# Kernel optimization log

Hardware: AMD Instinct MI355X
Metric: run time of the kernel (lower is better)

Reference implementation:

```python
import jax, jax.numpy as jnp
import numpy as np

B, S, D, H = 2, 2048, 1024, 16
HD = D // H  # head dim = 64


def setup_inputs() -> dict:
    key = jax.random.key(0)
    ks = jax.random.split(key, 8)
    s = 0.02
    return {
        "Q": jax.random.normal(ks[0], (B, S, D), jnp.float32),
        "K": jax.random.normal(ks[1], (B, S, D), jnp.float32),
        "V": jax.random.normal(ks[2], (B, S, D), jnp.float32),
        "mask": jax.random.randint(ks[3], (1, 1, S, S), 0, 2, jnp.int32),
        "Wq": jax.random.normal(ks[4], (D, D), jnp.float32) * s,
        "bq": jnp.zeros((D,), jnp.float32),
        "Wk": jax.random.normal(ks[5], (D, D), jnp.float32) * s,
        "bk": jnp.zeros((D,), jnp.float32),
        "Wv": jax.random.normal(ks[6], (D, D), jnp.float32) * s,
        "bv": jnp.zeros((D,), jnp.float32),
        "Wo": jax.random.normal(ks[7], (D, D), jnp.float32) * s,
        "bo": jnp.zeros((D,), jnp.float32),
    }


def reference(Q, K, V, mask, Wq, bq, Wk, bk, Wv, bv, Wo, bo):
    b = Q.shape[0]
    # QKV projections, split into heads: [B,S,D] -> [B,H,S,HD]
    q = (Q @ Wq + bq).reshape(b, -1, H, HD).transpose(0, 2, 1, 3)
    k = (K @ Wk + bk).reshape(b, -1, H, HD).transpose(0, 2, 1, 3)
    v = (V @ Wv + bv).reshape(b, -1, H, HD).transpose(0, 2, 1, 3)
    # scaled dot-product attention with full [B,H,S,S] scores (as in source)
    scale = jnp.sqrt(jnp.asarray(HD, q.dtype))
    scores = jnp.einsum("bhqd,bhkd->bhqk", q, k) / scale
    scores = jnp.where(mask == 0, -jnp.inf, scores)
    attn = jax.nn.softmax(scores, axis=-1)
    ctx = jnp.einsum("bhqk,bhkd->bhqd", attn, v)
    # merge heads and output projection
    concat = ctx.transpose(0, 2, 1, 3).reshape(b, -1, H * HD)
    return concat @ Wo + bo
```

## Files before the change

kernel.cpp:

```cpp
#include <hip/hip_runtime.h>


using s8v = __attribute__((ext_vector_type(8))) short;
using f4v = __attribute__((ext_vector_type(4))) float;
using f16v = __attribute__((ext_vector_type(16))) float;
typedef unsigned long long u64;

__device__ __forceinline__ unsigned short f2bf(float f) {
  union { float f; unsigned int u; } v; v.f = f;
  return (unsigned short)((v.u + 0x7fffu + ((v.u >> 16) & 1u)) >> 16);
}

__device__ __forceinline__ unsigned pkbf(float lo, float hi2) {
  return __builtin_amdgcn_perm(__float_as_uint(hi2), __float_as_uint(lo), 0x07060302);
}

__device__ __forceinline__ void gll16(const void* g, void* l) {
  __builtin_amdgcn_global_load_lds(
      (const __attribute__((address_space(1))) unsigned int*)g,
      (__attribute__((address_space(3))) unsigned int*)l, 16, 0, 0);
}

__global__ void prep_kernel(const float* __restrict__ Q, const float* __restrict__ K,
                            const float* __restrict__ V,
                            unsigned short* __restrict__ qb, unsigned short* __restrict__ kb,
                            unsigned short* __restrict__ vb,
                            const float* __restrict__ W0, const float* __restrict__ W1,
                            const float* __restrict__ W2, const float* __restrict__ W3,
                            unsigned short* __restrict__ T0, unsigned short* __restrict__ T1,
                            unsigned short* __restrict__ T2, unsigned short* __restrict__ T3,
                            const int* __restrict__ mask, unsigned* __restrict__ bmw) {
  __shared__ unsigned short t[64][72];
  const int bid = blockIdx.x, tid = threadIdx.x;
  if (bid < 12288) {
    int z = bid >> 12;
    int idx = (bid & 4095) * 256 + tid;
    const float* in = (z == 0) ? Q : (z == 1) ? K : V;
    unsigned short* out = (z == 0) ? qb : (z == 1) ? kb : vb;
    float4 v = ((const float4*)in)[idx];
    ushort4 o;
    o.x = f2bf(v.x); o.y = f2bf(v.y); o.z = f2bf(v.z); o.w = f2bf(v.w);
    ((ushort4*)out)[idx] = o;
  } else if (bid < 13312) {
    int b = bid - 12288;
    int z = b >> 8, rem = b & 255;
    int k0 = (rem >> 4) * 64, n0 = (rem & 15) * 64;
    const float* W = (z == 0) ? W0 : (z == 1) ? W1 : (z == 2) ? W2 : W3;
    unsigned short* Wt = (z == 0) ? T0 : (z == 1) ? T1 : (z == 2) ? T2 : T3;
    for (int p = 0; p < 4; ++p) {
      int idx = p * 256 + tid;
      int row = idx >> 4, c4 = idx & 15;
      float4 v = *(const float4*)&W[(size_t)(k0 + row) * 1024 + n0 + c4 * 4];
      t[row][c4 * 4 + 0] = f2bf(v.x);
      t[row][c4 * 4 + 1] = f2bf(v.y);
      t[row][c4 * 4 + 2] = f2bf(v.z);
      t[row][c4 * 4 + 3] = f2bf(v.w);
    }
    __syncthreads();
    for (int p = 0; p < 2; ++p) {
      int idx = p * 256 + tid;
      int j = idx >> 3, c8 = idx & 7;
      unsigned short tmp[8];
      for (int i = 0; i < 8; ++i) tmp[i] = t[c8 * 8 + i][j];
      uint4 o;
      o.x = tmp[0] | ((unsigned)tmp[1] << 16);
      o.y = tmp[2] | ((unsigned)tmp[3] << 16);
      o.z = tmp[4] | ((unsigned)tmp[5] << 16);
      o.w = tmp[6] | ((unsigned)tmp[7] << 16);
      *(uint4*)&Wt[(size_t)(n0 + j) * 1024 + k0 + c8 * 8] = o;
    }
  } else {
    int g = (bid - 13312) * 256 + tid;
    int widx = g & 15, hi = (g >> 4) & 1, l31 = (g >> 5) & 31;
    int it = (g >> 10) & 31, rowblk = g >> 15;
    int ni = widx >> 3, kcl = (widx >> 2) & 1, e = widx & 3;
    int kk = 64 * it + 32 * ni + 16 * kcl + 4 * hi + (e >> 1) * 8 + (e & 1) * 2;
    int qrow = rowblk * 32 + l31;
    const int* mrow = mask + (size_t)qrow * 2048 + kk;
    unsigned wd = (mrow[0] ? 0xFFFFu : 0u) | (mrow[1] ? 0xFFFF0000u : 0u);
    bmw[g] = wd;
  }
}

__global__ __launch_bounds__(256) void proj3_kernel(
    const unsigned short* __restrict__ A0, const unsigned short* __restrict__ A1,
    const unsigned short* __restrict__ A2,
    const unsigned short* __restrict__ W0, const unsigned short* __restrict__ W1,
    const unsigned short* __restrict__ W2,
    const float* __restrict__ b0, const float* __restrict__ b1, const float* __restrict__ b2,
    unsigned short* __restrict__ oq, unsigned short* __restrict__ ok,
    unsigned short* __restrict__ ovt) {
  const int z = blockIdx.z;
  const unsigned short* A  = (z == 0) ? A0 : (z == 1) ? A1 : A2;
  const unsigned short* Wt = (z == 0) ? W0 : (z == 1) ? W1 : W2;
  const float* bias        = (z == 0) ? b0 : (z == 1) ? b1 : b2;

  __shared__ __align__(16) unsigned short As[128 * 32];
  __shared__ __align__(16) unsigned short Bs[128 * 32];
  __shared__ __align__(16) unsigned short Ls[128][136];

  const int tid = threadIdx.x;
  const int lane = tid & 63, w = tid >> 6, ln = lane & 15, quad = lane >> 4;
  const int wm = (w & 1) * 64, wn = (w >> 1) * 64;
  const int m0 = blockIdx.x * 128, n0 = blockIdx.y * 128;

  const int slr = lane >> 2;
  const int schunk = (lane & 3) ^ ((lane >> 3) & 3);
  const int cfrag = (quad ^ ((ln >> 1) & 3)) * 8;

  f4v zero = {0.f, 0.f, 0.f, 0.f};
  f4v acc[4][4];
  for (int mi = 0; mi < 4; ++mi)
    for (int ni = 0; ni < 4; ++ni) acc[mi][ni] = zero;

  for (int kt = 0; kt < 1024; kt += 32) {
    __syncthreads();
    gll16(&A[(size_t)(m0 + w * 32 + slr) * 1024 + kt + schunk * 8],       &As[(w * 32) * 32]);
    gll16(&A[(size_t)(m0 + w * 32 + 16 + slr) * 1024 + kt + schunk * 8],  &As[(w * 32 + 16) * 32]);
    gll16(&Wt[(size_t)(n0 + w * 32 + slr) * 1024 + kt + schunk * 8],      &Bs[(w * 32) * 32]);
    gll16(&Wt[(size_t)(n0 + w * 32 + 16 + slr) * 1024 + kt + schunk * 8], &Bs[(w * 32 + 16) * 32]);
    __syncthreads();
    s8v a[4], b[4];
    for (int mi = 0; mi < 4; ++mi) a[mi] = *(const s8v*)&As[(wm + mi * 16 + ln) * 32 + cfrag];
    for (int ni = 0; ni < 4; ++ni) b[ni] = *(const s8v*)&Bs[(wn + ni * 16 + ln) * 32 + cfrag];
    if (z < 2) {
      for (int mi = 0; mi < 4; ++mi)
        for (int ni = 0; ni < 4; ++ni)
          acc[mi][ni] = __builtin_amdgcn_mfma_f32_16x16x32_bf16(a[mi], b[ni], acc[mi][ni], 0, 0, 0);
    } else {
      for (int mi = 0; mi < 4; ++mi)
        for (int ni = 0; ni < 4; ++ni)
          acc[mi][ni] = __builtin_amdgcn_mfma_f32_16x16x32_bf16(b[ni], a[mi], acc[mi][ni], 0, 0, 0);
    }
  }

  if (z < 2) {
    const float qscale = (z == 0) ? 0.18033688f : 1.0f;
    for (int mi = 0; mi < 4; ++mi) {
      int row = wm + mi * 16 + quad * 4;
      for (int ni = 0; ni < 4; ++ni) {
        int col = wn + ni * 16 + ln;
        float bvv = bias[n0 + col];
        for (int r = 0; r < 4; ++r)
          Ls[row + r][col] = f2bf((acc[mi][ni][r] + bvv) * qscale);
      }
    }
  } else {
    for (int ni = 0; ni < 4; ++ni) {
      for (int r = 0; r < 4; ++r) {
        int colw = wn + ni * 16 + quad * 4 + r;
        float bvv = bias[n0 + colw];
        for (int mi = 0; mi < 4; ++mi) {
          int rowg = wm + mi * 16 + ln;
          Ls[colw][rowg] = f2bf(acc[mi][ni][r] + bvv);
        }
      }
    }
  }
  __syncthreads();

  if (z < 2) {
    unsigned short* outp = (z == 0) ? oq : ok;
    for (int p = 0; p < 8; ++p) {
      int row = p * 16 + (tid >> 4);
      int cg  = tid & 15;
      uint4 vv = *(const uint4*)&Ls[row][cg * 8];
      int rb = m0 + row, b_ = rb >> 11, s = rb & 2047;
      int colg = n0 + cg * 8, h = colg >> 6, hd = colg & 63;
      *(uint4*)&outp[(((size_t)(b_ * 16 + h)) * 2048 + s) * 64 + hd] = vv;
    }
  } else {
    for (int p = 0; p < 8; ++p) {
      int rr = p * 16 + (tid >> 4);
      int cg = tid & 15;
      uint4 vv = *(const uint4*)&Ls[rr][cg * 8];
      int colw = n0 + rr, h = colw >> 6, hd = colw & 63;
      int sg = m0 + cg * 8, b_ = sg >> 11, ss = sg & 2047;
      *(uint4*)&ovt[(((size_t)(b_ * 16 + h)) * 64 + hd) * 2048 + ss] = vv;
    }
  }
}

#define FLASH_ITER(i, SIN0, SIN1, SOUT0, SOUT1)                                 \
  {                                                                             \
    const int cur = (i) & 1;                                                    \
    uint4 nA, nB, nC, nD;                                                       \
    if ((i) < 31) {                                                             \
      const uint4* m4 = (const uint4*)(mwp + ((i) + 1) * 1024);                 \
      nA = m4[0]; nB = m4[1]; nC = m4[2]; nD = m4[3];                           \
    }                                                                           \
          \
    __builtin_amdgcn_s_setprio(1);                                              \
    if ((i) < 31) {                                                             \
      s8v ak0 = *(const s8v*)&k_s[cur ^ 1][l31][hi * 8];                        \
      s8v ak1 = *(const s8v*)&k_s[cur ^ 1][32 + l31][hi * 8];                   \
      SOUT0 = __builtin_amdgcn_mfma_f32_32x32x16_bf16(ak0, qf[0], zf, 0, 0, 0); \
      SOUT1 = __builtin_amdgcn_mfma_f32_32x32x16_bf16(ak1, qf[0], zf, 0, 0, 0); \
      _Pragma("unroll")                                                         \
      for (int c = 1; c < 4; ++c) {                                             \
        ak0 = *(const s8v*)&k_s[cur ^ 1][l31][c * 16 + hi * 8];                 \
        ak1 = *(const s8v*)&k_s[cur ^ 1][32 + l31][c * 16 + hi * 8];            \
        SOUT0 = __builtin_amdgcn_mfma_f32_32x32x16_bf16(ak0, qf[c], SOUT0, 0, 0, 0); \
        SOUT1 = __builtin_amdgcn_mfma_f32_32x32x16_bf16(ak1, qf[c], SOUT1, 0, 0, 0); \
      }                                                                         \
    }                                                                           \
    __builtin_amdgcn_s_setprio(0);                                              \
         \
    s8v pf[4];                                                                  \
    _Pragma("unroll")                                                           \
    for (int ni = 0; ni < 2; ++ni) {                                            \
      const f16v sv = ni ? SIN1 : SIN0;                                         \
      _Pragma("unroll")                                                         \
      for (int kcl = 0; kcl < 2; ++kcl) {                                       \
        const int rb = 8 * kcl;                                                 \
        const uint4 mw = ni ? (kcl ? mwD : mwC) : (kcl ? mwB : mwA);            \
        unsigned x0 = pkbf(__builtin_amdgcn_exp2f(sv[rb + 0]),                  \
                           __builtin_amdgcn_exp2f(sv[rb + 1])) & mw.x;          \
        unsigned x1 = pkbf(__builtin_amdgcn_exp2f(sv[rb + 2]),                  \
                           __builtin_amdgcn_exp2f(sv[rb + 3])) & mw.y;          \
        unsigned y0 = pkbf(__builtin_amdgcn_exp2f(sv[rb + 4]),                  \
                           __builtin_amdgcn_exp2f(sv[rb + 5])) & mw.z;          \
        unsigned y1 = pkbf(__builtin_amdgcn_exp2f(sv[rb + 6]),                  \
                           __builtin_amdgcn_exp2f(sv[rb + 7])) & mw.w;          \
        asm("v_permlane32_swap_b32 %0, %1" : "+v"(x0), "+v"(y0));               \
        asm("v_permlane32_swap_b32 %0, %1" : "+v"(x1), "+v"(y1));               \
        union { uint4 u; s8v v; } cv;                                           \
        cv.u = make_uint4(x0, x1, y0, y1);                                      \
        pf[ni * 2 + kcl] = cv.v;                                                \
      }                                                                         \
    }                                                                           \
                                              \
    __builtin_amdgcn_s_setprio(1);                                              \
    _Pragma("unroll")                                                           \
    for (int kc = 0; kc < 4; ++kc)                                              \
      lac = __builtin_amdgcn_mfma_f32_32x32x16_bf16(pf[kc], ones, lac, 0, 0, 0);\
    _Pragma("unroll")                                                           \
    for (int kc = 0; kc < 4; ++kc) {                                            \
      s8v bv0 = *(const s8v*)&v_s[cur][l31][kc * 16 + hi * 8];                  \
      s8v bv1 = *(const s8v*)&v_s[cur][32 + l31][kc * 16 + hi * 8];             \
      o0 = __builtin_amdgcn_mfma_f32_32x32x16_bf16(pf[kc], bv0, o0, 0, 0, 0);   \
      o1 = __builtin_amdgcn_mfma_f32_32x32x16_bf16(pf[kc], bv1, o1, 0, 0, 0);   \
    }                                                                           \
    __builtin_amdgcn_s_setprio(0);                                              \
    __syncthreads();                             \
    if ((i) < 30) WRITET(cur);                         \
    if ((i) < 29) LOADT((i) + 3);                                               \
    __syncthreads();                      \
    mwA = nA; mwB = nB; mwC = nC; mwD = nD;                                     \
  }

__global__ __launch_bounds__(256, 2) void flash_kernel(
    const unsigned short* __restrict__ q, const unsigned short* __restrict__ k,
    const unsigned short* __restrict__ vt, const unsigned* __restrict__ bmw,
    unsigned short* __restrict__ ctx) {
  __shared__ __align__(16) unsigned short k_s[2][64][72];
  __shared__ __align__(16) unsigned short v_s[2][64][72];

  const int tid = threadIdx.x;
  const int lane = tid & 63, w = tid >> 6;
  const int l31 = lane & 31, hi = lane >> 5;
  const int q0 = blockIdx.x * 128;
  const int bh = blockIdx.y;
  const unsigned short* qg  = q  + ((size_t)bh * 2048 + q0) * 64;
  const unsigned short* kgb = k  + (size_t)bh * 2048 * 64;
  const unsigned short* vgb = vt + (size_t)bh * 64 * 2048;
  const unsigned* mwp = bmw + (size_t)(blockIdx.x * 4 + w) * 32768 + l31 * 32 + hi * 16;

  const int qrow = w * 32 + l31;
  s8v qf[4];
#pragma unroll
  for (int c = 0; c < 4; ++c)
    qf[c] = *(const s8v*)&qg[(size_t)qrow * 64 + c * 16 + hi * 8];

  s8v ones;
#pragma unroll
  for (int i = 0; i < 8; ++i) ones[i] = (short)0x3F80;
  f16v zf;
#pragma unroll
  for (int i = 0; i < 16; ++i) zf[i] = 0.f;

  const int srow = tid >> 3, sc8 = tid & 7;

  uint4 kr0, kr1, vr0, vr1;
  auto LOADT = [&](int it) {
    const int kk = it * 64;
    kr0 = *(const uint4*)&kgb[(size_t)(kk + srow) * 64 + sc8 * 8];
    kr1 = *(const uint4*)&kgb[(size_t)(kk + srow + 32) * 64 + sc8 * 8];
    vr0 = *(const uint4*)&vgb[(size_t)srow * 2048 + kk + sc8 * 8];
    vr1 = *(const uint4*)&vgb[(size_t)(srow + 32) * 2048 + kk + sc8 * 8];
  };
  auto WRITET = [&](int b) {
    *(uint4*)&k_s[b][srow][sc8 * 8] = kr0;
    *(uint4*)&k_s[b][srow + 32][sc8 * 8] = kr1;
    *(uint4*)&v_s[b][srow][sc8 * 8] = vr0;
    *(uint4*)&v_s[b][srow + 32][sc8 * 8] = vr1;
  };

  LOADT(0); WRITET(0);
  LOADT(1); WRITET(1);
  LOADT(2);
  __syncthreads();

  uint4 mwA, mwB, mwC, mwD;
  {
    const uint4* m4 = (const uint4*)mwp;
    mwA = m4[0]; mwB = m4[1]; mwC = m4[2]; mwD = m4[3];
  }

  f16v sA0, sA1, sB0, sB1;
  {
    s8v ak0 = *(const s8v*)&k_s[0][l31][hi * 8];
    s8v ak1 = *(const s8v*)&k_s[0][32 + l31][hi * 8];
    sA0 = __builtin_amdgcn_mfma_f32_32x32x16_bf16(ak0, qf[0], zf, 0, 0, 0);
    sA1 = __builtin_amdgcn_mfma_f32_32x32x16_bf16(ak1, qf[0], zf, 0, 0, 0);
#pragma unroll
    for (int c = 1; c < 4; ++c) {
      ak0 = *(const s8v*)&k_s[0][l31][c * 16 + hi * 8];
      ak1 = *(const s8v*)&k_s[0][32 + l31][c * 16 + hi * 8];
      sA0 = __builtin_amdgcn_mfma_f32_32x32x16_bf16(ak0, qf[c], sA0, 0, 0, 0);
      sA1 = __builtin_amdgcn_mfma_f32_32x32x16_bf16(ak1, qf[c], sA1, 0, 0, 0);
    }
  }

  f16v o0, o1, lac;
#pragma unroll
  for (int i = 0; i < 16; ++i) { o0[i] = 0.f; o1[i] = 0.f; lac[i] = 0.f; }

  for (int ii = 0; ii < 16; ++ii) {
    const int i0 = ii * 2;
    FLASH_ITER(i0,     sA0, sA1, sB0, sB1);
    FLASH_ITER(i0 + 1, sB0, sB1, sA0, sA1);
  }

  const int b_ = bh >> 4, h = bh & 15;
#pragma unroll
  for (int r = 0; r < 16; ++r) {
    const int ql = (r & 3) + 8 * (r >> 2) + 4 * hi;
    const float inv = 1.f / lac[r];
    const int srw = q0 + w * 32 + ql;
    const size_t base = ((size_t)b_ * 2048 + srw) * 1024 + h * 64;
    ctx[base + l31] = f2bf(o0[r] * inv);
    ctx[base + 32 + l31] = f2bf(o1[r] * inv);
  }
}

__global__ __launch_bounds__(256) void gemm_out_kernel(
    const unsigned short* __restrict__ A, const unsigned short* __restrict__ Wt,
    const float* __restrict__ bias, float* __restrict__ out) {
  __shared__ __align__(16) unsigned short As[128 * 32];
  __shared__ __align__(16) unsigned short Bs[128 * 32];

  const int tid = threadIdx.x;
  const int lane = tid & 63, w = tid >> 6, ln = lane & 15, quad = lane >> 4;
  const int wm = (w & 1) * 64, wn = (w >> 1) * 64;
  const int m0 = blockIdx.x * 128, n0 = blockIdx.y * 128;

  const int slr = lane >> 2;
  const int schunk = (lane & 3) ^ ((lane >> 3) & 3);
  const int cfrag = (quad ^ ((ln >> 1) & 3)) * 8;

  f4v zero = {0.f, 0.f, 0.f, 0.f};
  f4v acc[4][4];
  for (int mi = 0; mi < 4; ++mi)
    for (int ni = 0; ni < 4; ++ni) acc[mi][ni] = zero;

  for (int kt = 0; kt < 1024; kt += 32) {
    __syncthreads();
    gll16(&A[(size_t)(m0 + w * 32 + slr) * 1024 + kt + schunk * 8],       &As[(w * 32) * 32]);
    gll16(&A[(size_t)(m0 + w * 32 + 16 + slr) * 1024 + kt + schunk * 8],  &As[(w * 32 + 16) * 32]);
    gll16(&Wt[(size_t)(n0 + w * 32 + slr) * 1024 + kt + schunk * 8],      &Bs[(w * 32) * 32]);
    gll16(&Wt[(size_t)(n0 + w * 32 + 16 + slr) * 1024 + kt + schunk * 8], &Bs[(w * 32 + 16) * 32]);
    __syncthreads();
    s8v a[4], b[4];
    for (int mi = 0; mi < 4; ++mi) a[mi] = *(const s8v*)&As[(wm + mi * 16 + ln) * 32 + cfrag];
    for (int ni = 0; ni < 4; ++ni) b[ni] = *(const s8v*)&Bs[(wn + ni * 16 + ln) * 32 + cfrag];
    for (int mi = 0; mi < 4; ++mi)
      for (int ni = 0; ni < 4; ++ni)
        acc[mi][ni] = __builtin_amdgcn_mfma_f32_16x16x32_bf16(a[mi], b[ni], acc[mi][ni], 0, 0, 0);
  }

  for (int mi = 0; mi < 4; ++mi) {
    int rb = m0 + wm + mi * 16 + quad * 4;
    for (int ni = 0; ni < 4; ++ni) {
      int col = n0 + wn + ni * 16 + ln;
      float bvv = bias[col];
      for (int r = 0; r < 4; ++r)
        out[(size_t)(rb + r) * 1024 + col] = acc[mi][ni][r] + bvv;
    }
  }
}

extern "C" void kernel_launch(void* const* d_in, const int* in_sizes, int n_in,
                              void* d_out, int out_size, void* d_ws, size_t ws_size,
                              hipStream_t stream) {
  const float* Q  = (const float*)d_in[0];
  const float* K  = (const float*)d_in[1];
  const float* V  = (const float*)d_in[2];
  const int* mask = (const int*)d_in[3];
  const float* Wq = (const float*)d_in[4];
  const float* bq = (const float*)d_in[5];
  const float* Wk = (const float*)d_in[6];
  const float* bk = (const float*)d_in[7];
  const float* Wv = (const float*)d_in[8];
  const float* bv = (const float*)d_in[9];
  const float* Wo = (const float*)d_in[10];
  const float* bo = (const float*)d_in[11];
  float* out = (float*)d_out;

  char* ws = (char*)d_ws;
  const size_t MB = 1u << 20;
  unsigned short* qb  = (unsigned short*)(ws + 0 * MB);
  unsigned short* kb  = (unsigned short*)(ws + 8 * MB);
  unsigned short* vb  = (unsigned short*)(ws + 16 * MB);
  unsigned short* wqt = (unsigned short*)(ws + 24 * MB);
  unsigned short* wkt = (unsigned short*)(ws + 26 * MB);
  unsigned short* wvt = (unsigned short*)(ws + 28 * MB);
  unsigned short* wot = (unsigned short*)(ws + 30 * MB);
  unsigned short* qh  = (unsigned short*)(ws + 32 * MB);
  unsigned short* kh  = (unsigned short*)(ws + 40 * MB);
  unsigned short* vth = (unsigned short*)(ws + 48 * MB);
  unsigned* bmw       = (unsigned*)(ws + 56 * MB);
  unsigned short* ctx = (unsigned short*)(ws + 16 * MB);

  prep_kernel<<<21504, 256, 0, stream>>>(Q, K, V, qb, kb, vb,
                                         Wq, Wk, Wv, Wo, wqt, wkt, wvt, wot,
                                         mask, bmw);
  proj3_kernel<<<dim3(32, 8, 3), 256, 0, stream>>>(qb, kb, vb, wqt, wkt, wvt,
                                                   bq, bk, bv, qh, kh, vth);
  flash_kernel<<<dim3(16, 32), 256, 0, stream>>>(qh, kh, vth, bmw, ctx);
  gemm_out_kernel<<<dim3(32, 8), 256, 0, stream>>>(ctx, wot, bo, out);
}
```

Baseline: 246.1 us.

## Load K/V MFMA fragments directly from global into registers, drop LDS staging

Measured after the change: 344.0 us. 1.4x slower.

```diff
diff --git a/kernel.cpp b/kernel.cpp
--- a/kernel.cpp
+++ b/kernel.cpp
@@ -183,29 +183,25 @@
 
 #define FLASH_ITER(i, SIN0, SIN1, SOUT0, SOUT1)                                 \
   {                                                                             \
-    const int cur = (i) & 1;                                                    \
     uint4 nA, nB, nC, nD;                                                       \
     if ((i) < 31) {                                                             \
       const uint4* m4 = (const uint4*)(mwp + ((i) + 1) * 1024);                 \
       nA = m4[0]; nB = m4[1]; nC = m4[2]; nD = m4[3];                           \
     }                                                                           \
-          \
+             \
     __builtin_amdgcn_s_setprio(1);                                              \
     if ((i) < 31) {                                                             \
-      s8v ak0 = *(const s8v*)&k_s[cur ^ 1][l31][hi * 8];                        \
-      s8v ak1 = *(const s8v*)&k_s[cur ^ 1][32 + l31][hi * 8];                   \
-      SOUT0 = __builtin_amdgcn_mfma_f32_32x32x16_bf16(ak0, qf[0], zf, 0, 0, 0); \
-      SOUT1 = __builtin_amdgcn_mfma_f32_32x32x16_bf16(ak1, qf[0], zf, 0, 0, 0); \
+      SOUT0 = __builtin_amdgcn_mfma_f32_32x32x16_bf16(kf0[0], qf[0], zf, 0, 0, 0); \
+      SOUT1 = __builtin_amdgcn_mfma_f32_32x32x16_bf16(kf1[0], qf[0], zf, 0, 0, 0); \
       _Pragma("unroll")                                                         \
       for (int c = 1; c < 4; ++c) {                                             \
-        ak0 = *(const s8v*)&k_s[cur ^ 1][l31][c * 16 + hi * 8];                 \
-        ak1 = *(const s8v*)&k_s[cur ^ 1][32 + l31][c * 16 + hi * 8];            \
-        SOUT0 = __builtin_amdgcn_mfma_f32_32x32x16_bf16(ak0, qf[c], SOUT0, 0, 0, 0); \
-        SOUT1 = __builtin_amdgcn_mfma_f32_32x32x16_bf16(ak1, qf[c], SOUT1, 0, 0, 0); \
+        SOUT0 = __builtin_amdgcn_mfma_f32_32x32x16_bf16(kf0[c], qf[c], SOUT0, 0, 0, 0); \
+        SOUT1 = __builtin_amdgcn_mfma_f32_32x32x16_bf16(kf1[c], qf[c], SOUT1, 0, 0, 0); \
       }                                                                         \
     }                                                                           \
     __builtin_amdgcn_s_setprio(0);                                              \
-         \
+    if ((i) < 30) LK((i) + 2);     \
+        \
     s8v pf[4];                                                                  \
     _Pragma("unroll")                                                           \
     for (int ni = 0; ni < 2; ++ni) {                                            \
@@ -229,23 +225,18 @@
         pf[ni * 2 + kcl] = cv.v;                                                \
       }                                                                         \
     }                                                                           \
-                                              \
+           \
     __builtin_amdgcn_s_setprio(1);                                              \
     _Pragma("unroll")                                                           \
     for (int kc = 0; kc < 4; ++kc)                                              \
       lac = __builtin_amdgcn_mfma_f32_32x32x16_bf16(pf[kc], ones, lac, 0, 0, 0);\
     _Pragma("unroll")                                                           \
     for (int kc = 0; kc < 4; ++kc) {                                            \
-      s8v bv0 = *(const s8v*)&v_s[cur][l31][kc * 16 + hi * 8];                  \
-      s8v bv1 = *(const s8v*)&v_s[cur][32 + l31][kc * 16 + hi * 8];             \
-      o0 = __builtin_amdgcn_mfma_f32_32x32x16_bf16(pf[kc], bv0, o0, 0, 0, 0);   \
-      o1 = __builtin_amdgcn_mfma_f32_32x32x16_bf16(pf[kc], bv1, o1, 0, 0, 0);   \
+      o0 = __builtin_amdgcn_mfma_f32_32x32x16_bf16(pf[kc], vf0[kc], o0, 0, 0, 0); \
+      o1 = __builtin_amdgcn_mfma_f32_32x32x16_bf16(pf[kc], vf1[kc], o1, 0, 0, 0); \
     }                                                                           \
     __builtin_amdgcn_s_setprio(0);                                              \
-    __syncthreads();                             \
-    if ((i) < 30) WRITET(cur);                         \
-    if ((i) < 29) LOADT((i) + 3);                                               \
-    __syncthreads();                      \
+    if ((i) < 31) LV((i) + 1);     \
     mwA = nA; mwB = nB; mwC = nC; mwD = nD;                                     \
   }
 
@@ -253,9 +244,6 @@
     const unsigned short* __restrict__ q, const unsigned short* __restrict__ k,
     const unsigned short* __restrict__ vt, const unsigned* __restrict__ bmw,
     unsigned short* __restrict__ ctx) {
-  __shared__ __align__(16) unsigned short k_s[2][64][72];
-  __shared__ __align__(16) unsigned short v_s[2][64][72];
-
   const int tid = threadIdx.x;
   const int lane = tid & 63, w = tid >> 6;
   const int l31 = lane & 31, hi = lane >> 5;
@@ -279,47 +267,45 @@
 #pragma unroll
   for (int i = 0; i < 16; ++i) zf[i] = 0.f;
 
-  const int srow = tid >> 3, sc8 = tid & 7;
-
-  uint4 kr0, kr1, vr0, vr1;
-  auto LOADT = [&](int it) {
-    const int kk = it * 64;
-    kr0 = *(const uint4*)&kgb[(size_t)(kk + srow) * 64 + sc8 * 8];
-    kr1 = *(const uint4*)&kgb[(size_t)(kk + srow + 32) * 64 + sc8 * 8];
-    vr0 = *(const uint4*)&vgb[(size_t)srow * 2048 + kk + sc8 * 8];
-    vr1 = *(const uint4*)&vgb[(size_t)(srow + 32) * 2048 + kk + sc8 * 8];
+  const unsigned short* kp0 = kgb + (size_t)l31 * 64 + hi * 8;
+  const unsigned short* kp1 = kgb + (size_t)(32 + l31) * 64 + hi * 8;
+  const unsigned short* vp0 = vgb + (size_t)l31 * 2048 + hi * 8;
+  const unsigned short* vp1 = vgb + (size_t)(32 + l31) * 2048 + hi * 8;
+
+  s8v kf0[4], kf1[4], vf0[4], vf1[4];
+  auto LK = [&](int it) {
+    const size_t off = (size_t)it * 4096;
+#pragma unroll
+    for (int c = 0; c < 4; ++c) {
+      kf0[c] = *(const s8v*)&kp0[off + c * 16];
+      kf1[c] = *(const s8v*)&kp1[off + c * 16];
+    }
   };
-  auto WRITET = [&](int b) {
-    *(uint4*)&k_s[b][srow][sc8 * 8] = kr0;
-    *(uint4*)&k_s[b][srow + 32][sc8 * 8] = kr1;
-    *(uint4*)&v_s[b][srow][sc8 * 8] = vr0;
-    *(uint4*)&v_s[b][srow + 32][sc8 * 8] = vr1;
+  auto LV = [&](int it) {
+    const int off = it * 64;
+#pragma unroll
+    for (int c = 0; c < 4; ++c) {
+      vf0[c] = *(const s8v*)&vp0[off + c * 16];
+      vf1[c] = *(const s8v*)&vp1[off + c * 16];
+    }
   };
 
-  LOADT(0); WRITET(0);
-  LOADT(1); WRITET(1);
-  LOADT(2);
-  __syncthreads();
+  LK(0);
+  f16v sA0, sA1, sB0, sB1;
+  sA0 = __builtin_amdgcn_mfma_f32_32x32x16_bf16(kf0[0], qf[0], zf, 0, 0, 0);
+  sA1 = __builtin_amdgcn_mfma_f32_32x32x16_bf16(kf1[0], qf[0], zf, 0, 0, 0);
+#pragma unroll
+  for (int c = 1; c < 4; ++c) {
+    sA0 = __builtin_amdgcn_mfma_f32_32x32x16_bf16(kf0[c], qf[c], sA0, 0, 0, 0);
+    sA1 = __builtin_amdgcn_mfma_f32_32x32x16_bf16(kf1[c], qf[c], sA1, 0, 0, 0);
+  }
+  LK(1);
+  LV(0);
 
   uint4 mwA, mwB, mwC, mwD;
   {
     const uint4* m4 = (const uint4*)mwp;
     mwA = m4[0]; mwB = m4[1]; mwC = m4[2]; mwD = m4[3];
-  }
-
-  f16v sA0, sA1, sB0, sB1;
-  {
-    s8v ak0 = *(const s8v*)&k_s[0][l31][hi * 8];
-    s8v ak1 = *(const s8v*)&k_s[0][32 + l31][hi * 8];
-    sA0 = __builtin_amdgcn_mfma_f32_32x32x16_bf16(ak0, qf[0], zf, 0, 0, 0);
-    sA1 = __builtin_amdgcn_mfma_f32_32x32x16_bf16(ak1, qf[0], zf, 0, 0, 0);
-#pragma unroll
-    for (int c = 1; c < 4; ++c) {
-      ak0 = *(const s8v*)&k_s[0][l31][c * 16 + hi * 8];
-      ak1 = *(const s8v*)&k_s[0][32 + l31][c * 16 + hi * 8];
-      sA0 = __builtin_amdgcn_mfma_f32_32x32x16_bf16(ak0, qf[c], sA0, 0, 0, 0);
-      sA1 = __builtin_amdgcn_mfma_f32_32x32x16_bf16(ak1, qf[c], sA1, 0, 0, 0);
-    }
   }
 
   f16v o0, o1, lac;
```

## Fuse fp32-to-bf16 activation conversion into QKV projection and move mask packing

Applied to the files above, without the earlier changes.

After: 272.3 us. +10.6%, slower.

```diff
diff --git a/kernel.cpp b/kernel.cpp
--- a/kernel.cpp
+++ b/kernel.cpp
@@ -11,6 +11,12 @@
   return (unsigned short)((v.u + 0x7fffu + ((v.u >> 16) & 1u)) >> 16);
 }
 
+__device__ __forceinline__ unsigned cvtpk(float a, float b) {
+  unsigned r;
+  asm("v_cvt_pk_bf16_f32 %0, %1, %2" : "=v"(r) : "v"(a), "v"(b));
+  return r;
+}
+
 __device__ __forceinline__ unsigned pkbf(float lo, float hi2) {
   return __builtin_amdgcn_perm(__float_as_uint(hi2), __float_as_uint(lo), 0x07060302);
 }
@@ -21,77 +27,69 @@
       (__attribute__((address_space(3))) unsigned int*)l, 16, 0, 0);
 }
 
-__global__ void prep_kernel(const float* __restrict__ Q, const float* __restrict__ K,
-                            const float* __restrict__ V,
-                            unsigned short* __restrict__ qb, unsigned short* __restrict__ kb,
-                            unsigned short* __restrict__ vb,
-                            const float* __restrict__ W0, const float* __restrict__ W1,
+__global__ void prep_kernel(const float* __restrict__ W0, const float* __restrict__ W1,
                             const float* __restrict__ W2, const float* __restrict__ W3,
                             unsigned short* __restrict__ T0, unsigned short* __restrict__ T1,
-                            unsigned short* __restrict__ T2, unsigned short* __restrict__ T3,
-                            const int* __restrict__ mask, unsigned* __restrict__ bmw) {
+                            unsigned short* __restrict__ T2, unsigned short* __restrict__ T3) {
   __shared__ unsigned short t[64][72];
   const int bid = blockIdx.x, tid = threadIdx.x;
-  if (bid < 12288) {
-    int z = bid >> 12;
-    int idx = (bid & 4095) * 256 + tid;
-    const float* in = (z == 0) ? Q : (z == 1) ? K : V;
-    unsigned short* out = (z == 0) ? qb : (z == 1) ? kb : vb;
-    float4 v = ((const float4*)in)[idx];
-    ushort4 o;
-    o.x = f2bf(v.x); o.y = f2bf(v.y); o.z = f2bf(v.z); o.w = f2bf(v.w);
-    ((ushort4*)out)[idx] = o;
-  } else if (bid < 13312) {
-    int b = bid - 12288;
-    int z = b >> 8, rem = b & 255;
-    int k0 = (rem >> 4) * 64, n0 = (rem & 15) * 64;
-    const float* W = (z == 0) ? W0 : (z == 1) ? W1 : (z == 2) ? W2 : W3;
-    unsigned short* Wt = (z == 0) ? T0 : (z == 1) ? T1 : (z == 2) ? T2 : T3;
-    for (int p = 0; p < 4; ++p) {
-      int idx = p * 256 + tid;
-      int row = idx >> 4, c4 = idx & 15;
-      float4 v = *(const float4*)&W[(size_t)(k0 + row) * 1024 + n0 + c4 * 4];
-      t[row][c4 * 4 + 0] = f2bf(v.x);
-      t[row][c4 * 4 + 1] = f2bf(v.y);
-      t[row][c4 * 4 + 2] = f2bf(v.z);
-      t[row][c4 * 4 + 3] = f2bf(v.w);
-    }
-    __syncthreads();
-    for (int p = 0; p < 2; ++p) {
-      int idx = p * 256 + tid;
-      int j = idx >> 3, c8 = idx & 7;
-      unsigned short tmp[8];
-      for (int i = 0; i < 8; ++i) tmp[i] = t[c8 * 8 + i][j];
-      uint4 o;
-      o.x = tmp[0] | ((unsigned)tmp[1] << 16);
-      o.y = tmp[2] | ((unsigned)tmp[3] << 16);
-      o.z = tmp[4] | ((unsigned)tmp[5] << 16);
-      o.w = tmp[6] | ((unsigned)tmp[7] << 16);
-      *(uint4*)&Wt[(size_t)(n0 + j) * 1024 + k0 + c8 * 8] = o;
-    }
-  } else {
-    int g = (bid - 13312) * 256 + tid;
-    int widx = g & 15, hi = (g >> 4) & 1, l31 = (g >> 5) & 31;
-    int it = (g >> 10) & 31, rowblk = g >> 15;
-    int ni = widx >> 3, kcl = (widx >> 2) & 1, e = widx & 3;
-    int kk = 64 * it + 32 * ni + 16 * kcl + 4 * hi + (e >> 1) * 8 + (e & 1) * 2;
-    int qrow = rowblk * 32 + l31;
-    const int* mrow = mask + (size_t)qrow * 2048 + kk;
-    unsigned wd = (mrow[0] ? 0xFFFFu : 0u) | (mrow[1] ? 0xFFFF0000u : 0u);
-    bmw[g] = wd;
+  int z = bid >> 8, rem = bid & 255;
+  int k0 = (rem >> 4) * 64, n0 = (rem & 15) * 64;
+  const float* W = (z == 0) ? W0 : (z == 1) ? W1 : (z == 2) ? W2 : W3;
+  unsigned short* Wt = (z == 0) ? T0 : (z == 1) ? T1 : (z == 2) ? T2 : T3;
+  for (int p = 0; p < 4; ++p) {
+    int idx = p * 256 + tid;
+    int row = idx >> 4, c4 = idx & 15;
+    float4 v = *(const float4*)&W[(size_t)(k0 + row) * 1024 + n0 + c4 * 4];
+    t[row][c4 * 4 + 0] = f2bf(v.x);
+    t[row][c4 * 4 + 1] = f2bf(v.y);
+    t[row][c4 * 4 + 2] = f2bf(v.z);
+    t[row][c4 * 4 + 3] = f2bf(v.w);
+  }
+  __syncthreads();
+  for (int p = 0; p < 2; ++p) {
+    int idx = p * 256 + tid;
+    int j = idx >> 3, c8 = idx & 7;
+    unsigned short tmp[8];
+    for (int i = 0; i < 8; ++i) tmp[i] = t[c8 * 8 + i][j];
+    uint4 o;
+    o.x = tmp[0] | ((unsigned)tmp[1] << 16);
+    o.y = tmp[2] | ((unsigned)tmp[3] << 16);
+    o.z = tmp[4] | ((unsigned)tmp[5] << 16);
+    o.w = tmp[6] | ((unsigned)tmp[7] << 16);
+    *(uint4*)&Wt[(size_t)(n0 + j) * 1024 + k0 + c8 * 8] = o;
   }
 }
 
 __global__ __launch_bounds__(256) void proj3_kernel(
-    const unsigned short* __restrict__ A0, const unsigned short* __restrict__ A1,
-    const unsigned short* __restrict__ A2,
+    const float* __restrict__ A0, const float* __restrict__ A1,
+    const float* __restrict__ A2,
     const unsigned short* __restrict__ W0, const unsigned short* __restrict__ W1,
     const unsigned short* __restrict__ W2,
     const float* __restrict__ b0, const float* __restrict__ b1, const float* __restrict__ b2,
     unsigned short* __restrict__ oq, unsigned short* __restrict__ ok,
-    unsigned short* __restrict__ ovt) {
+    unsigned short* __restrict__ ovt,
+    const int* __restrict__ mask, unsigned* __restrict__ bmw) {
   const int z = blockIdx.z;
-  const unsigned short* A  = (z == 0) ? A0 : (z == 1) ? A1 : A2;
+  const int tid = threadIdx.x;
+
+  if (z == 3) {
+    const int idx = blockIdx.y * 32 + blockIdx.x;
+    for (int j = 0; j < 32; ++j) {
+      int g = idx * 256 + tid + j * 65536;
+      int widx = g & 15, hi = (g >> 4) & 1, l31 = (g >> 5) & 31;
+      int it = (g >> 10) & 31, rowblk = g >> 15;
+      int ni = widx >> 3, kcl = (widx >> 2) & 1, e = widx & 3;
+      int kk = 64 * it + 32 * ni + 16 * kcl + 4 * hi + (e >> 1) * 8 + (e & 1) * 2;
+      int qrow = rowblk * 32 + l31;
+      const int* mrow = mask + (size_t)qrow * 2048 + kk;
+      unsigned wd = (mrow[0] ? 0xFFFFu : 0u) | (mrow[1] ? 0xFFFF0000u : 0u);
+      bmw[g] = wd;
+    }
+    return;
+  }
+
+  const float* A = (z == 0) ? A0 : (z == 1) ? A1 : A2;
   const unsigned short* Wt = (z == 0) ? W0 : (z == 1) ? W1 : W2;
   const float* bias        = (z == 0) ? b0 : (z == 1) ? b1 : b2;
 
@@ -99,7 +97,6 @@
   __shared__ __align__(16) unsigned short Bs[128 * 32];
   __shared__ __align__(16) unsigned short Ls[128][136];
 
-  const int tid = threadIdx.x;
   const int lane = tid & 63, w = tid >> 6, ln = lane & 15, quad = lane >> 4;
   const int wm = (w & 1) * 64, wn = (w >> 1) * 64;
   const int m0 = blockIdx.x * 128, n0 = blockIdx.y * 128;
@@ -107,6 +104,10 @@
   const int slr = lane >> 2;
   const int schunk = (lane & 3) ^ ((lane >> 3) & 3);
   const int cfrag = (quad ^ ((ln >> 1) & 3)) * 8;
+
+  const int ar = tid >> 2, ac = tid & 3;
+  const int asw = (ar >> 1) & 3;
+  const int acg = (ac ^ asw) * 8;
 
   f4v zero = {0.f, 0.f, 0.f, 0.f};
   f4v acc[4][4];
@@ -115,10 +116,20 @@
 
   for (int kt = 0; kt < 1024; kt += 32) {
     __syncthreads();
-    gll16(&A[(size_t)(m0 + w * 32 + slr) * 1024 + kt + schunk * 8],       &As[(w * 32) * 32]);
-    gll16(&A[(size_t)(m0 + w * 32 + 16 + slr) * 1024 + kt + schunk * 8],  &As[(w * 32 + 16) * 32]);
     gll16(&Wt[(size_t)(n0 + w * 32 + slr) * 1024 + kt + schunk * 8],      &Bs[(w * 32) * 32]);
     gll16(&Wt[(size_t)(n0 + w * 32 + 16 + slr) * 1024 + kt + schunk * 8], &Bs[(w * 32 + 16) * 32]);
+    {
+      const float* p0 = &A[(size_t)(m0 + ar) * 1024 + kt + acg];
+      const float* p1 = &A[(size_t)(m0 + ar + 64) * 1024 + kt + acg];
+      float4 f0a = *(const float4*)p0, f0b = *(const float4*)(p0 + 4);
+      float4 f1a = *(const float4*)p1, f1b = *(const float4*)(p1 + 4);
+      *(uint4*)&As[ar * 32 + ac * 8] =
+          make_uint4(cvtpk(f0a.x, f0a.y), cvtpk(f0a.z, f0a.w),
+                     cvtpk(f0b.x, f0b.y), cvtpk(f0b.z, f0b.w));
+      *(uint4*)&As[(ar + 64) * 32 + ac * 8] =
+          make_uint4(cvtpk(f1a.x, f1a.y), cvtpk(f1a.z, f1a.w),
+                     cvtpk(f1b.x, f1b.y), cvtpk(f1b.z, f1b.w));
+    }
     __syncthreads();
     s8v a[4], b[4];
     for (int mi = 0; mi < 4; ++mi) a[mi] = *(const s8v*)&As[(wm + mi * 16 + ln) * 32 + cfrag];
@@ -409,9 +420,6 @@
 
   char* ws = (char*)d_ws;
   const size_t MB = 1u << 20;
-  unsigned short* qb  = (unsigned short*)(ws + 0 * MB);
-  unsigned short* kb  = (unsigned short*)(ws + 8 * MB);
-  unsigned short* vb  = (unsigned short*)(ws + 16 * MB);
   unsigned short* wqt = (unsigned short*)(ws + 24 * MB);
   unsigned short* wkt = (unsigned short*)(ws + 26 * MB);
   unsigned short* wvt = (unsigned short*)(ws + 28 * MB);
@@ -422,11 +430,10 @@
   unsigned* bmw       = (unsigned*)(ws + 56 * MB);
   unsigned short* ctx = (unsigned short*)(ws + 16 * MB);
 
-  prep_kernel<<<21504, 256, 0, stream>>>(Q, K, V, qb, kb, vb,
-                                         Wq, Wk, Wv, Wo, wqt, wkt, wvt, wot,
-                                         mask, bmw);
-  proj3_kernel<<<dim3(32, 8, 3), 256, 0, stream>>>(qb, kb, vb, wqt, wkt, wvt,
-                                                   bq, bk, bv, qh, kh, vth);
+  prep_kernel<<<1024, 256, 0, stream>>>(Wq, Wk, Wv, Wo, wqt, wkt, wvt, wot);
+  proj3_kernel<<<dim3(32, 8, 4), 256, 0, stream>>>(Q, K, V, wqt, wkt, wvt,
+                                                   bq, bk, bv, qh, kh, vth,
+                                                   mask, bmw);
   flash_kernel<<<dim3(16, 32), 256, 0, stream>>>(qh, kh, vth, bmw, ctx);
   gemm_out_kernel<<<dim3(32, 8), 256, 0, stream>>>(ctx, wot, bo, out);
 }
```
